# Performance work log

Hardware: AMD Instinct MI355X
Metric: run time of the kernel (lower is better)

Reference implementation:

```python
import jax, jax.numpy as jnp
import numpy as np

EPS = 1e-05  # eigenvalue clamp, from module __init__ default


def setup_inputs() -> dict:
    key = jax.random.key(0)
    B, C = 8192, 64
    A = jax.random.normal(key, (B, C, C), dtype=jnp.float32)
    # Build well-conditioned SPD matrices: S = A A^T / C + 1e-3 I
    S = jnp.einsum('bij,bkj->bik', A, A) / C + 1e-3 * jnp.eye(C, dtype=jnp.float32)
    return {"S": S}


def reference(S) -> jnp.ndarray:
    """Log-Euclidean map: S = Q diag(w) Q^T -> Q diag(log(max(w, eps))) Q^T.

    Faithful to SPDLogMap.forward: compute in float32, clamp eigenvalues at eps,
    cast result back to the input dtype.
    """
    orig_dtype = S.dtype
    Sf = S.astype(jnp.float32)
    w, v = jnp.linalg.eigh(Sf)                      # w: (B, C), v: (B, C, C)
    log_w = jnp.log(jnp.maximum(w, EPS))            # clamp then log
    # Q diag(log_w) Q^T without materializing diag_embed
    result = jnp.einsum('bic,bc,bjc->bij', v, log_w, v)
    return result.astype(orig_dtype)
```

## Files before the change

### kernel.cpp

```cpp
#include <hip/hip_runtime.h>
#include <math.h>

#define NSWEEP_MAX 16
#define T2_TOL 1e-8f
#define EPS2 1e-10f


template <int CTRL>
__device__ __forceinline__ int dpp1(int x) {
    return __builtin_amdgcn_update_dpp(0, x, CTRL, 0xF, 0xF, true);
}
__device__ __forceinline__ float dppf(float x, int) = delete;
template <int CTRL>
__device__ __forceinline__ float dppf1(float x) {
    return __int_as_float(dpp1<CTRL>(__float_as_int(x)));
}
__device__ __forceinline__ float swap16_self(float x) {
    asm("v_permlane16_swap_b32 %0, %0" : "+v"(x));
    return x;
}
__device__ __forceinline__ float swap32_self(float x) {
    asm("v_permlane32_swap_b32 %0, %0" : "+v"(x));
    return x;
}
__device__ __forceinline__ float rdlane_f(float x, int l) {
    return __int_as_float(__builtin_amdgcn_readlane(__float_as_int(x), l));
}

#define DPP_X1 0xB1
#define DPP_X2 0x4E
#define DPP_X3 0x1B
#define DPP_X7 0x141
#define DPP_X8 0x128

__global__ __launch_bounds__(64, 2) void spdlog_onesided(
    const float* __restrict__ S, float* __restrict__ Out, int nmat) {
    __shared__ float X[64][64];
    const int lane = threadIdx.x;
    const int b = blockIdx.x;
    if (b >= nmat) return;
    const float* Sb = S + (size_t)b * 4096;
    float* Ob = Out + (size_t)b * 4096;

    float g[64];
    #pragma unroll 64
    for (int s = 0; s < 64; ++s) g[s] = Sb[s * 64 + lane];

    float dpp = 0.0f;

    #pragma unroll 1
    for (int sweep = 0; sweep < NSWEEP_MAX; ++sweep) {
        float d0 = 0.0f, d1 = 0.0f, d2 = 0.0f, d3 = 0.0f;
        #pragma unroll 16
        for (int s = 0; s < 64; s += 4) {
            d0 = fmaf(g[s], g[s], d0);
            d1 = fmaf(g[s + 1], g[s + 1], d1);
            d2 = fmaf(g[s + 2], g[s + 2], d2);
            d3 = fmaf(g[s + 3], g[s + 3], d3);
        }
        dpp = (d0 + d1) + (d2 + d3);

        float pr[64];
        #pragma unroll 64
        for (int s = 0; s < 64; ++s) pr[s] = dppf1<DPP_X1>(g[s]);
        float pd = dppf1<DPP_X1>(dpp);

        float maxt2 = 0.0f;
        #pragma unroll 1
        for (int i = 1; i < 64; ++i) {
            if (i > 1) {
                const int delta = i & (-i);
                switch (delta) {
                    case 1:
                        #pragma unroll
                        for (int s = 0; s < 64; ++s) pr[s] = dppf1<DPP_X1>(pr[s]);
                        pd = dppf1<DPP_X1>(pd);
                        break;
                    case 2:
                        #pragma unroll
                        for (int s = 0; s < 64; ++s) pr[s] = dppf1<DPP_X2>(pr[s]);
                        pd = dppf1<DPP_X2>(pd);
                        break;
                    case 4:
                        #pragma unroll
                        for (int s = 0; s < 64; ++s)
                            pr[s] = dppf1<DPP_X7>(dppf1<DPP_X3>(pr[s]));
                        pd = dppf1<DPP_X7>(dppf1<DPP_X3>(pd));
                        break;
                    case 8:
                        #pragma unroll
                        for (int s = 0; s < 64; ++s) pr[s] = dppf1<DPP_X8>(pr[s]);
                        pd = dppf1<DPP_X8>(pd);
                        break;
                    case 16:
                        #pragma unroll
                        for (int s = 0; s < 64; ++s) pr[s] = swap16_self(pr[s]);
                        pd = swap16_self(pd);
                        break;
                    default:
                        #pragma unroll
                        for (int s = 0; s < 64; ++s) pr[s] = swap32_self(pr[s]);
                        pd = swap32_self(pd);
                        break;
                }
            }
            const int m = i ^ (i >> 1);
            const int xl = lane ^ m;
            const bool isLow = lane < xl;
            float a0 = 0.0f, a1 = 0.0f, a2 = 0.0f, a3 = 0.0f;
            #pragma unroll 16
            for (int s = 0; s < 64; s += 4) {
                a0 = fmaf(g[s], pr[s], a0);
                a1 = fmaf(g[s + 1], pr[s + 1], a1);
                a2 = fmaf(g[s + 2], pr[s + 2], a2);
                a3 = fmaf(g[s + 3], pr[s + 3], a3);
            }
            const float dpq = (a0 + a1) + (a2 + a3);
            const float t2 = dpq * dpq * __builtin_amdgcn_rcpf(dpp * pd);
            maxt2 = fmaxf(maxt2, t2);
            if (__all(t2 < T2_TOL)) continue;
            const float d_lo = isLow ? dpp : pd;
            const float d_hi = isLow ? pd : dpp;
            const float tau = (d_hi - d_lo) * __builtin_amdgcn_rcpf(2.0f * dpq);
            const float sq = __builtin_amdgcn_sqrtf(fmaf(tau, tau, 1.0f));
            float tt = __builtin_amdgcn_rcpf(fabsf(tau) + sq);
            tt = copysignf(tt, tau);
            float cc = __builtin_amdgcn_rsqf(fmaf(tt, tt, 1.0f));
            float ss = tt * cc;
            const bool tiny = fabsf(dpq) < 1e-30f;
            cc = tiny ? 1.0f : cc;
            ss = tiny ? 0.0f : ss;
            tt = tiny ? 0.0f : tt;
            const float es = isLow ? -ss : ss;
            const float t_own = isLow ? tt : -tt;
            const float pdn = fmaf(t_own, dpq, pd);
            dpp = fmaf(-t_own, dpq, dpp);
            pd = pdn;
            #pragma unroll 64
            for (int s = 0; s < 64; ++s) {
                const float m1 = es * pr[s];
                const float m2 = es * g[s];
                g[s] = fmaf(cc, g[s], m1);
                pr[s] = fmaf(cc, pr[s], -m2);
            }
        }
        maxt2 = fmaxf(maxt2, __shfl_xor(maxt2, 1));
        maxt2 = fmaxf(maxt2, __shfl_xor(maxt2, 2));
        maxt2 = fmaxf(maxt2, __shfl_xor(maxt2, 4));
        maxt2 = fmaxf(maxt2, __shfl_xor(maxt2, 8));
        maxt2 = fmaxf(maxt2, __shfl_xor(maxt2, 16));
        maxt2 = fmaxf(maxt2, __shfl_xor(maxt2, 32));
        if (maxt2 < T2_TOL) break;
    }

    float dfin = 0.0f;
    #pragma unroll 64
    for (int s = 0; s < 64; ++s) dfin = fmaf(g[s], g[s], dfin);
    const float w = 0.5f * logf(fmaxf(dfin, EPS2));
    const float rs = __builtin_amdgcn_rsqf(fmaxf(dfin, 1e-20f));

    #pragma unroll 64
    for (int s = 0; s < 64; ++s) X[s][lane] = g[s] * rs;
    __syncthreads();
    float uw[64];
    {
        const float4* rowp = (const float4*)&X[lane][0];
        #pragma unroll 16
        for (int gq = 0; gq < 16; ++gq) {
            const float4 q = rowp[gq];
            uw[4 * gq + 0] = q.x;
            uw[4 * gq + 1] = q.y;
            uw[4 * gq + 2] = q.z;
            uw[4 * gq + 3] = q.w;
        }
    }
    #pragma unroll 64
    for (int c = 0; c < 64; ++c) uw[c] *= rdlane_f(w, c);
    #pragma unroll 2
    for (int i = 0; i < 64; ++i) {
        const float4* Urow = (const float4*)&X[i][0];
        float acc = 0.0f;
        #pragma unroll 16
        for (int gq = 0; gq < 16; ++gq) {
            const float4 q = Urow[gq];
            acc = fmaf(q.x, uw[4 * gq + 0], acc);
            acc = fmaf(q.y, uw[4 * gq + 1], acc);
            acc = fmaf(q.z, uw[4 * gq + 2], acc);
            acc = fmaf(q.w, uw[4 * gq + 3], acc);
        }
        Ob[i * 64 + lane] = acc;
    }
}

extern "C" void kernel_launch(void* const* d_in, const int* in_sizes, int n_in,
                              void* d_out, int out_size, void* d_ws, size_t ws_size,
                              hipStream_t stream) {
    const float* S = (const float*)d_in[0];
    float* Out = (float*)d_out;
    const int nmat = in_sizes[0] / 4096;
    spdlog_onesided<<<nmat, 64, 0, stream>>>(S, Out, nmat);
}
```

Baseline: 4.317 ms.

## Split each matrix's rows across two wavefronts with LDS partial-dot exchange

Each block now uses two wavefronts, each holding 32 rows of the 64-column working matrix, so per-thread register arrays shrink from 64 to 32 floats. Column norms and pairwise dot products are computed as partial sums and combined through shared memory, which adds a __syncthreads barrier to every Jacobi rotation step. The aim is lower register pressure, higher occupancy and more parallel work per matrix. The cost is about 63 extra block barriers per sweep plus LDS traffic on the critical path.

```diff
diff --git a/kernel.cpp b/kernel.cpp
--- a/kernel.cpp
+++ b/kernel.cpp
@@ -10,7 +10,6 @@
 __device__ __forceinline__ int dpp1(int x) {
     return __builtin_amdgcn_update_dpp(0, x, CTRL, 0xF, 0xF, true);
 }
-__device__ __forceinline__ float dppf(float x, int) = delete;
 template <int CTRL>
 __device__ __forceinline__ float dppf1(float x) {
     return __int_as_float(dpp1<CTRL>(__float_as_int(x)));
@@ -33,36 +32,48 @@
 #define DPP_X7 0x141
 #define DPP_X8 0x128
 
-__global__ __launch_bounds__(64, 2) void spdlog_onesided(
+__global__ __launch_bounds__(128, 2) void spdlog_onesided2(
     const float* __restrict__ S, float* __restrict__ Out, int nmat) {
     __shared__ float X[64][64];
-    const int lane = threadIdx.x;
+    const int tid = threadIdx.x;
+    const int lane = tid & 63;
+    const int wv = tid >> 6;
+    const int rbase = wv << 5;
     const int b = blockIdx.x;
     if (b >= nmat) return;
     const float* Sb = S + (size_t)b * 4096;
     float* Ob = Out + (size_t)b * 4096;
 
-    float g[64];
-    #pragma unroll 64
-    for (int s = 0; s < 64; ++s) g[s] = Sb[s * 64 + lane];
+    float g[32];
+    #pragma unroll 32
+    for (int s = 0; s < 32; ++s) g[s] = Sb[(rbase + s) * 64 + lane];
 
     float dpp = 0.0f;
 
     #pragma unroll 1
     for (int sweep = 0; sweep < NSWEEP_MAX; ++sweep) {
-        float d0 = 0.0f, d1 = 0.0f, d2 = 0.0f, d3 = 0.0f;
-        #pragma unroll 16
-        for (int s = 0; s < 64; s += 4) {
-            d0 = fmaf(g[s], g[s], d0);
-            d1 = fmaf(g[s + 1], g[s + 1], d1);
-            d2 = fmaf(g[s + 2], g[s + 2], d2);
-            d3 = fmaf(g[s + 3], g[s + 3], d3);
-        }
-        dpp = (d0 + d1) + (d2 + d3);
-
-        float pr[64];
-        #pragma unroll 64
-        for (int s = 0; s < 64; ++s) pr[s] = dppf1<DPP_X1>(g[s]);
+        {
+            float d0 = 0.0f, d1 = 0.0f, d2 = 0.0f, d3 = 0.0f;
+            #pragma unroll 8
+            for (int s = 0; s < 32; s += 4) {
+                d0 = fmaf(g[s], g[s], d0);
+                d1 = fmaf(g[s + 1], g[s + 1], d1);
+                d2 = fmaf(g[s + 2], g[s + 2], d2);
+                d3 = fmaf(g[s + 3], g[s + 3], d3);
+            }
+            const float own = (d0 + d1) + (d2 + d3);
+            __syncthreads();
+            X[4 + wv][lane] = own;
+            __syncthreads();
+            const float oth = X[4 + (1 ^ wv)][lane];
+            const float p0 = wv ? oth : own;
+            const float p1 = wv ? own : oth;
+            dpp = p0 + p1;
+        }
+
+        float pr[32];
+        #pragma unroll 32
+        for (int s = 0; s < 32; ++s) pr[s] = dppf1<DPP_X1>(g[s]);
         float pd = dppf1<DPP_X1>(dpp);
 
         float maxt2 = 0.0f;
@@ -73,33 +84,33 @@
                 switch (delta) {
                     case 1:
                         #pragma unroll
-                        for (int s = 0; s < 64; ++s) pr[s] = dppf1<DPP_X1>(pr[s]);
+                        for (int s = 0; s < 32; ++s) pr[s] = dppf1<DPP_X1>(pr[s]);
                         pd = dppf1<DPP_X1>(pd);
                         break;
                     case 2:
                         #pragma unroll
-                        for (int s = 0; s < 64; ++s) pr[s] = dppf1<DPP_X2>(pr[s]);
+                        for (int s = 0; s < 32; ++s) pr[s] = dppf1<DPP_X2>(pr[s]);
                         pd = dppf1<DPP_X2>(pd);
                         break;
                     case 4:
                         #pragma unroll
-                        for (int s = 0; s < 64; ++s)
+                        for (int s = 0; s < 32; ++s)
                             pr[s] = dppf1<DPP_X7>(dppf1<DPP_X3>(pr[s]));
                         pd = dppf1<DPP_X7>(dppf1<DPP_X3>(pd));
                         break;
                     case 8:
                         #pragma unroll
-                        for (int s = 0; s < 64; ++s) pr[s] = dppf1<DPP_X8>(pr[s]);
+                        for (int s = 0; s < 32; ++s) pr[s] = dppf1<DPP_X8>(pr[s]);
                         pd = dppf1<DPP_X8>(pd);
                         break;
                     case 16:
                         #pragma unroll
-                        for (int s = 0; s < 64; ++s) pr[s] = swap16_self(pr[s]);
+                        for (int s = 0; s < 32; ++s) pr[s] = swap16_self(pr[s]);
                         pd = swap16_self(pd);
                         break;
                     default:
                         #pragma unroll
-                        for (int s = 0; s < 64; ++s) pr[s] = swap32_self(pr[s]);
+                        for (int s = 0; s < 32; ++s) pr[s] = swap32_self(pr[s]);
                         pd = swap32_self(pd);
                         break;
                 }
@@ -108,14 +119,21 @@
             const int xl = lane ^ m;
             const bool isLow = lane < xl;
             float a0 = 0.0f, a1 = 0.0f, a2 = 0.0f, a3 = 0.0f;
-            #pragma unroll 16
-            for (int s = 0; s < 64; s += 4) {
+            #pragma unroll 8
+            for (int s = 0; s < 32; s += 4) {
                 a0 = fmaf(g[s], pr[s], a0);
                 a1 = fmaf(g[s + 1], pr[s + 1], a1);
                 a2 = fmaf(g[s + 2], pr[s + 2], a2);
                 a3 = fmaf(g[s + 3], pr[s + 3], a3);
             }
-            const float dpq = (a0 + a1) + (a2 + a3);
+            const float own = (a0 + a1) + (a2 + a3);
+            const int pbuf = (i & 1) << 1;
+            X[pbuf + wv][lane] = own;
+            __syncthreads();
+            const float oth = X[pbuf + (1 ^ wv)][lane];
+            const float p0 = wv ? oth : own;
+            const float p1 = wv ? own : oth;
+            const float dpq = p0 + p1;
             const float t2 = dpq * dpq * __builtin_amdgcn_rcpf(dpp * pd);
             maxt2 = fmaxf(maxt2, t2);
             if (__all(t2 < T2_TOL)) continue;
@@ -136,8 +154,8 @@
             const float pdn = fmaf(t_own, dpq, pd);
             dpp = fmaf(-t_own, dpq, dpp);
             pd = pdn;
-            #pragma unroll 64
-            for (int s = 0; s < 64; ++s) {
+            #pragma unroll 32
+            for (int s = 0; s < 32; ++s) {
                 const float m1 = es * pr[s];
                 const float m2 = es * g[s];
                 g[s] = fmaf(cc, g[s], m1);
@@ -153,14 +171,29 @@
         if (maxt2 < T2_TOL) break;
     }
 
-    float dfin = 0.0f;
-    #pragma unroll 64
-    for (int s = 0; s < 64; ++s) dfin = fmaf(g[s], g[s], dfin);
+    float dfin;
+    {
+        float d0 = 0.0f, d1 = 0.0f;
+        #pragma unroll 16
+        for (int s = 0; s < 32; s += 2) {
+            d0 = fmaf(g[s], g[s], d0);
+            d1 = fmaf(g[s + 1], g[s + 1], d1);
+        }
+        const float own = d0 + d1;
+        __syncthreads();
+        X[4 + wv][lane] = own;
+        __syncthreads();
+        const float oth = X[4 + (1 ^ wv)][lane];
+        const float p0 = wv ? oth : own;
+        const float p1 = wv ? own : oth;
+        dfin = p0 + p1;
+    }
     const float w = 0.5f * logf(fmaxf(dfin, EPS2));
     const float rs = __builtin_amdgcn_rsqf(fmaxf(dfin, 1e-20f));
 
-    #pragma unroll 64
-    for (int s = 0; s < 64; ++s) X[s][lane] = g[s] * rs;
+    __syncthreads();
+    #pragma unroll 32
+    for (int s = 0; s < 32; ++s) X[rbase + s][lane] = g[s] * rs;
     __syncthreads();
     float uw[64];
     {
@@ -177,7 +210,8 @@
     #pragma unroll 64
     for (int c = 0; c < 64; ++c) uw[c] *= rdlane_f(w, c);
     #pragma unroll 2
-    for (int i = 0; i < 64; ++i) {
+    for (int ii = 0; ii < 32; ++ii) {
+        const int i = rbase + ii;
         const float4* Urow = (const float4*)&X[i][0];
         float acc = 0.0f;
         #pragma unroll 16
@@ -198,5 +232,5 @@
     const float* S = (const float*)d_in[0];
     float* Out = (float*)d_out;
     const int nmat = in_sizes[0] / 4096;
-    spdlog_onesided<<<nmat, 64, 0, stream>>>(S, Out, nmat);
-}
+    spdlog_onesided2<<<nmat, 128, 0, stream>>>(S, Out, nmat);
+}
```

New measurement: 6.314 ms. 46.3% more time.
